# Kernel tuning notes

Measured on AMD Instinct MI355X. Metric: run time of the kernel, lower is better.

Reference implementation:

```python
import jax, jax.numpy as jnp
import numpy as np

# Module hyperparameters (from init_kwargs)
THRESHOLD = 1.0
TAU_MEM = 20.0
TAU_ADP = 200.0
BETA = 0.1          # adaptive-threshold coupling
SG_BETA = 10.0      # fast_sigmoid surrogate slope
ALPHA_MEM = float(np.exp(-1.0 / TAU_MEM))
ALPHA_ADP = float(np.exp(-1.0 / TAU_ADP))


@jax.custom_vjp
def spike_fn(u):
    # SpikingFunction.forward: (input >= threshold).float()
    return (u >= THRESHOLD).astype(u.dtype)

def _spike_fwd(u):
    return spike_fn(u), u

def _spike_bwd(u, g):
    # fast_sigmoid surrogate on (input - threshold)
    return (g / (1.0 + jnp.abs(SG_BETA * (u - THRESHOLD))),)

spike_fn.defvjp(_spike_fwd, _spike_bwd)


def setup_inputs() -> dict:
    key = jax.random.key(0)
    x = jax.random.normal(key, (32, 512, 1024), dtype=jnp.float32)  # [B, T, D]
    return {"x": x}


def reference(x):
    B = x.shape[0]
    state_shape = (B,) + x.shape[2:]
    v0 = jnp.zeros(state_shape, dtype=x.dtype)  # membrane potential
    a0 = jnp.zeros(state_shape, dtype=x.dtype)  # adaptive threshold

    def step(carry, x_t):
        v, a = carry
        v = ALPHA_MEM * v + x_t
        cur_thr = THRESHOLD + BETA * a
        # NOTE: original passes (v - cur_thr) into a spike fn that itself
        # compares against THRESHOLD, so the threshold counts twice.
        s = spike_fn(v - cur_thr)
        a = ALPHA_ADP * a + s
        v = v - s * THRESHOLD  # reset == 'subtract'
        return (v, a), s

    x_tmajor = jnp.swapaxes(x, 0, 1)  # [T, B, D]
    _, spikes = jax.lax.scan(step, (v0, a0), x_tmajor)
    return jnp.swapaxes(spikes, 0, 1)  # [B, T, D]
```

## Files before the change

kernel.cpp:

```cpp
#include <hip/hip_runtime.h>


#define T_STEPS 512
#define D_DIM   1024

#define ALPHA_MEM 0.9512294245007141f
#define ALPHA_ADP 0.9950124791926823f

__device__ __forceinline__ bool adlif_step(float xv, float& v, float& a) {
    v = __fadd_rn(__fmul_rn(ALPHA_MEM, v), xv);
    float cur = __fadd_rn(1.0f, __fmul_rn(0.1f, a));
    float u = __fsub_rn(v, cur);
    bool fired = (u >= 1.0f);
    float s = fired ? 1.0f : 0.0f;
    a = __fadd_rn(__fmul_rn(ALPHA_ADP, a), s);
    v = __fsub_rn(v, s);
    return fired;
}

__global__ __launch_bounds__(64) void adlif_kernel(const float* __restrict__ x,
                                                   float* __restrict__ out) {
    __shared__ unsigned sbits[64 * 17];

    const int tid = threadIdx.x;
    const int idx = blockIdx.x * 64 + tid;
    const int b = idx >> 10;
    const int d = idx & (D_DIM - 1);
    const size_t base = (size_t)b * (T_STEPS * D_DIM) + d;
    const float* xp = x + base;
    float* op = out + base;

    float v = 0.0f, a = 0.0f;

    constexpr int U = 32;
    float buf0[U], buf1[U];

#pragma unroll
    for (int i = 0; i < U; ++i) buf0[i] = xp[i * D_DIM];

    for (int it = 0; it < T_STEPS / (2 * U); ++it) {
        const int t0 = it * 2 * U;

#pragma unroll
        for (int i = 0; i < U; ++i) buf1[i] = xp[(t0 + U + i) * D_DIM];

        unsigned wA = 0u;
#pragma unroll
        for (int i = 0; i < U; ++i) {
            bool f = adlif_step(buf0[i], v, a);
            wA |= ((unsigned)f) << i;
        }
        sbits[tid * 17 + it * 2] = wA;

        if (it + 1 < T_STEPS / (2 * U)) {
#pragma unroll
            for (int i = 0; i < U; ++i) buf0[i] = xp[(t0 + 2 * U + i) * D_DIM];
        }

        unsigned wB = 0u;
#pragma unroll
        for (int i = 0; i < U; ++i) {
            bool f = adlif_step(buf1[i], v, a);
            wB |= ((unsigned)f) << i;
        }
        sbits[tid * 17 + it * 2 + 1] = wB;
    }

    for (int w = 0; w < T_STEPS / 32; ++w) {
        const unsigned wb = sbits[tid * 17 + w];
#pragma unroll
        for (int k = 0; k < 32; ++k) {
            float s = (float)((wb >> k) & 1u);
            __builtin_nontemporal_store(s, &op[(size_t)(w * 32 + k) * D_DIM]);
        }
    }
}

extern "C" void kernel_launch(void* const* d_in, const int* in_sizes, int n_in,
                              void* d_out, int out_size, void* d_ws, size_t ws_size,
                              hipStream_t stream) {
    const float* x = (const float*)d_in[0];
    float* out = (float*)d_out;

    const int total = in_sizes[0];
    const int channels = total / T_STEPS;
    const int blocks = channels / 64;

    adlif_kernel<<<blocks, 64, 0, stream>>>(x, out);
}
```

Measured before the change: 30.90 us.

## Split scan and spike expansion into two kernels via workspace bitmask

The recurrence kernel now only scans and writes packed spike bits to a global workspace. A second, wide kernel expands the bits into float spikes with vectorized 16-byte nontemporal stores, using 256-thread blocks. The scan's unroll buffer doubles to 64 steps, which raises register pressure. The original single-kernel path is kept as a fallback when the workspace is too small, and the split adds a second launch plus a small round trip through the workspace.

```diff
diff --git a/kernel.cpp b/kernel.cpp
--- a/kernel.cpp
+++ b/kernel.cpp
@@ -3,9 +3,12 @@
 
 #define T_STEPS 512
 #define D_DIM   1024
+#define N_CHAN  32768
 
 #define ALPHA_MEM 0.9512294245007141f
 #define ALPHA_ADP 0.9950124791926823f
+
+typedef float f32x4 __attribute__((ext_vector_type(4)));
 
 __device__ __forceinline__ bool adlif_step(float xv, float& v, float& a) {
     v = __fadd_rn(__fmul_rn(ALPHA_MEM, v), xv);
@@ -18,21 +21,17 @@
     return fired;
 }
 
-__global__ __launch_bounds__(64) void adlif_kernel(const float* __restrict__ x,
-                                                   float* __restrict__ out) {
-    __shared__ unsigned sbits[64 * 17];
-
-    const int tid = threadIdx.x;
-    const int idx = blockIdx.x * 64 + tid;
+__global__ __launch_bounds__(64) void adlif_scan(const float* __restrict__ x,
+                                                 unsigned* __restrict__ wsbits) {
+    const int idx = blockIdx.x * 64 + threadIdx.x;
     const int b = idx >> 10;
     const int d = idx & (D_DIM - 1);
     const size_t base = (size_t)b * (T_STEPS * D_DIM) + d;
     const float* xp = x + base;
-    float* op = out + base;
 
     float v = 0.0f, a = 0.0f;
 
-    constexpr int U = 32;
+    constexpr int U = 64;
     float buf0[U], buf1[U];
 
 #pragma unroll
@@ -44,28 +43,88 @@
 #pragma unroll
         for (int i = 0; i < U; ++i) buf1[i] = xp[(t0 + U + i) * D_DIM];
 
-        unsigned wA = 0u;
+        unsigned wA0 = 0u, wA1 = 0u;
 #pragma unroll
         for (int i = 0; i < U; ++i) {
             bool f = adlif_step(buf0[i], v, a);
-            wA |= ((unsigned)f) << i;
+            if (i < 32) wA0 |= ((unsigned)f) << i;
+            else        wA1 |= ((unsigned)f) << (i - 32);
         }
-        sbits[tid * 17 + it * 2] = wA;
+        wsbits[(it * 4 + 0) * N_CHAN + idx] = wA0;
+        wsbits[(it * 4 + 1) * N_CHAN + idx] = wA1;
 
         if (it + 1 < T_STEPS / (2 * U)) {
 #pragma unroll
             for (int i = 0; i < U; ++i) buf0[i] = xp[(t0 + 2 * U + i) * D_DIM];
         }
 
-        unsigned wB = 0u;
+        unsigned wB0 = 0u, wB1 = 0u;
 #pragma unroll
         for (int i = 0; i < U; ++i) {
             bool f = adlif_step(buf1[i], v, a);
-            wB |= ((unsigned)f) << i;
+            if (i < 32) wB0 |= ((unsigned)f) << i;
+            else        wB1 |= ((unsigned)f) << (i - 32);
         }
+        wsbits[(it * 4 + 2) * N_CHAN + idx] = wB0;
+        wsbits[(it * 4 + 3) * N_CHAN + idx] = wB1;
+    }
+}
+
+__global__ __launch_bounds__(256) void adlif_expand(const unsigned* __restrict__ wsbits,
+                                                    float* __restrict__ out) {
+    const int b = blockIdx.x >> 4;
+    const int w = blockIdx.x & 15;
+    const int d0 = threadIdx.x * 4;
+    const int c0 = (b << 10) + d0;
+
+    const uint4 wd = *reinterpret_cast<const uint4*>(&wsbits[(size_t)w * N_CHAN + c0]);
+
+    float* op = out + ((size_t)b * T_STEPS + w * 32) * D_DIM + d0;
+
+#pragma unroll
+    for (int k = 0; k < 32; ++k) {
+        f32x4 val;
+        val.x = (float)((wd.x >> k) & 1u);
+        val.y = (float)((wd.y >> k) & 1u);
+        val.z = (float)((wd.z >> k) & 1u);
+        val.w = (float)((wd.w >> k) & 1u);
+        __builtin_nontemporal_store(val, (f32x4*)(op + (size_t)k * D_DIM));
+    }
+}
+
+__global__ __launch_bounds__(64) void adlif_single(const float* __restrict__ x,
+                                                   float* __restrict__ out) {
+    __shared__ unsigned sbits[64 * 17];
+    const int tid = threadIdx.x;
+    const int idx = blockIdx.x * 64 + tid;
+    const int b = idx >> 10;
+    const int d = idx & (D_DIM - 1);
+    const size_t base = (size_t)b * (T_STEPS * D_DIM) + d;
+    const float* xp = x + base;
+    float* op = out + base;
+
+    float v = 0.0f, a = 0.0f;
+    constexpr int U = 32;
+    float buf0[U], buf1[U];
+#pragma unroll
+    for (int i = 0; i < U; ++i) buf0[i] = xp[i * D_DIM];
+    for (int it = 0; it < T_STEPS / (2 * U); ++it) {
+        const int t0 = it * 2 * U;
+#pragma unroll
+        for (int i = 0; i < U; ++i) buf1[i] = xp[(t0 + U + i) * D_DIM];
+        unsigned wA = 0u;
+#pragma unroll
+        for (int i = 0; i < U; ++i) { bool f = adlif_step(buf0[i], v, a); wA |= ((unsigned)f) << i; }
+        sbits[tid * 17 + it * 2] = wA;
+        if (it + 1 < T_STEPS / (2 * U)) {
+#pragma unroll
+            for (int i = 0; i < U; ++i) buf0[i] = xp[(t0 + 2 * U + i) * D_DIM];
+        }
+        unsigned wB = 0u;
+#pragma unroll
+        for (int i = 0; i < U; ++i) { bool f = adlif_step(buf1[i], v, a); wB |= ((unsigned)f) << i; }
         sbits[tid * 17 + it * 2 + 1] = wB;
     }
-
     for (int w = 0; w < T_STEPS / 32; ++w) {
         const unsigned wb = sbits[tid * 17 + w];
 #pragma unroll
@@ -82,9 +141,13 @@
     const float* x = (const float*)d_in[0];
     float* out = (float*)d_out;
 
-    const int total = in_sizes[0];
-    const int channels = total / T_STEPS;
-    const int blocks = channels / 64;
+    const size_t need = (size_t)N_CHAN * (T_STEPS / 32) * sizeof(unsigned);
 
-    adlif_kernel<<<blocks, 64, 0, stream>>>(x, out);
+    if (ws_size >= need) {
+        unsigned* wsbits = (unsigned*)d_ws;
+        adlif_scan<<<N_CHAN / 64, 64, 0, stream>>>(x, wsbits);
+        adlif_expand<<<32 * 16, 256, 0, stream>>>(wsbits, out);
+    } else {
+        adlif_single<<<N_CHAN / 64, 64, 0, stream>>>(x, out);
+    }
 }
```

Result: slower. 36.11 us (+16.8%).
